# Performance work log

Measured on AMD Instinct MI355X. Metric: run time of the kernel, lower is better.

The kernel has to match this reference:

```python
import jax, jax.numpy as jnp
from jax import lax
import numpy as np

N_LAYER = 2
SEQ, BATCH, D = 4096, 32, 512


def setup_inputs() -> dict:
    key = jax.random.key(0)
    k1, k2, k3 = jax.random.split(key, 3)
    x = jax.random.normal(k1, (SEQ, BATCH, D), dtype=jnp.float32)
    # repo init: weight_ih ~ N(0, 0.01)
    W_ih = jax.random.normal(k2, (N_LAYER, D, D), dtype=jnp.float32) * 0.01
    # recurrent weight in [0,1) keeps the long ReLU recurrence bounded
    w_hh = jax.random.uniform(k3, (N_LAYER, D), dtype=jnp.float32)
    b_ih = jnp.zeros((N_LAYER, D), dtype=jnp.float32)
    return {"x": x, "W_ih": W_ih, "w_hh": w_hh, "b_ih": b_ih}


def _indrnn_layer(x, W, w, b):
    # x: (T, B, in), W: (H, in), w,b: (H,)
    proj = jnp.einsum('tbi,hi->tbh', x, W) + b  # one batched GEMM up front

    def step(h, p):
        h = jax.nn.relu(p + w * h)
        return h, h

    h0 = jnp.zeros((x.shape[1], W.shape[0]), dtype=x.dtype)
    hT, ys = lax.scan(step, h0, proj)
    return ys, hT


def reference(x, W_ih, w_hh, b_ih):
    hiddens = []
    out = x
    for l in range(W_ih.shape[0]):  # small fixed layer loop
        out, hT = _indrnn_layer(out, W_ih[l], w_hh[l], b_ih[l])
        hiddens.append(hT)
    h_n = jnp.stack(hiddens, axis=0)  # (n_layer, B, H)
    return out, h_n
```

## Files before the change

### kernel.cpp

```cpp
#include <hip/hip_runtime.h>

#define T_SEQ   4096
#define BATCH   32
#define DIM     512
#define MROWS   (T_SEQ * BATCH)
#define S_STRIDE (BATCH * DIM)
#define OUT_ELEMS ((size_t)T_SEQ * BATCH * DIM)
#define NCH     32
#define CLEN    (T_SEQ / NCH)
#define NCHAIN  (BATCH * DIM)

#define GNWG    ((MROWS / 256) * (DIM / 256))
#define OFF_A0  0
#define OFF_A1  16384
#define OFF_B0  32768
#define OFF_B1  49152
#define GLDS_B  131072

typedef __bf16 bf8_t __attribute__((ext_vector_type(8)));
typedef float  f4_t  __attribute__((ext_vector_type(4)));
typedef unsigned short u16x8 __attribute__((ext_vector_type(8)));
typedef __attribute__((address_space(1))) void gvoid_t;
typedef __attribute__((address_space(3))) void lvoid_t;

__device__ __forceinline__ unsigned short f2bf(float f) {
    unsigned int u = __float_as_uint(f);
    u += 0x7FFFu + ((u >> 16) & 1u);
    return (unsigned short)(u >> 16);
}
__device__ __forceinline__ float bf2f(unsigned short b) {
    return __uint_as_float(((unsigned int)b) << 16);
}

#define VMC(n)  asm volatile("s_waitcnt vmcnt(" #n ")" ::: "memory")
#define LGKM0   asm volatile("s_waitcnt lgkmcnt(0)" ::: "memory")
#define PH_PRE()  do { __builtin_amdgcn_s_barrier(); LGKM0;                    \
                       __builtin_amdgcn_sched_barrier(0);                      \
                       __builtin_amdgcn_s_setprio(1); } while (0)
#define PH_POST() do { __builtin_amdgcn_s_setprio(0);                          \
                       __builtin_amdgcn_sched_barrier(0);                      \
                       __builtin_amdgcn_s_barrier(); } while (0)

__global__ __launch_bounds__(256) void k_cvt(const float* __restrict__ in,
                                             unsigned short* __restrict__ out) {
    size_t i = ((size_t)blockIdx.x * 256 + threadIdx.x) * 8;
    float4 a = *reinterpret_cast<const float4*>(in + i);
    float4 b = *reinterpret_cast<const float4*>(in + i + 4);
    u16x8 o;
    o[0] = f2bf(a.x); o[1] = f2bf(a.y); o[2] = f2bf(a.z); o[3] = f2bf(a.w);
    o[4] = f2bf(b.x); o[5] = f2bf(b.y); o[6] = f2bf(b.z); o[7] = f2bf(b.w);
    *reinterpret_cast<u16x8*>(out + i) = o;
}

template <int AF32>
__global__ __launch_bounds__(512, 2)
void k_gemm8(const void* __restrict__ Ap,
             const unsigned short* __restrict__ Bp,
             unsigned short* __restrict__ C) {
    extern __shared__ unsigned short lds[];

    const int tid  = threadIdx.x;
    const int lane = tid & 63;
    const int wv   = tid >> 6;
    const int wr   = wv >> 2;
    const int wc   = wv & 3;
    const int l15  = lane & 15;
    const int l16  = lane >> 4;
    const int lj   = lane >> 3;
    const int ss8  = lane & 7;

    const int sid = (blockIdx.x & 7) * (GNWG / 8) + (blockIdx.x >> 3);
    const size_t gm = (size_t)(sid >> 1) * 256;
    const int    gn = (sid & 1) * 256;

    const unsigned short* Ab = (const unsigned short*)Ap;
    const float*          Af = (const float*)Ap;

    auto stage = [&](const unsigned short* gbase, size_t grow0, int region,
                     int half, int kt) {
#pragma unroll
        for (int j = 0; j < 2; ++j) {
            const int r = half * 128 + j * 64 + wv * 8 + lj;
            const unsigned short* src =
                gbase + (grow0 + r) * 512 + kt * 64 + ((ss8 ^ (r & 7)) * 8);
            unsigned short* dst = &lds[region + half * 8192 + j * 4096 + wv * 512];
            __builtin_amdgcn_global_load_lds((gvoid_t*)src, (lvoid_t*)dst, 16, 0, 0);
        }
    };
    auto loadAf = [&](float4* h, int half, int kt) {
#pragma unroll
        for (int j = 0; j < 2; ++j) {
            const int r = half * 128 + j * 64 + wv * 8 + lj;
            const float* src = Af + (gm + r) * 512 + kt * 64 + ss8 * 8;
            h[j * 2]     = *reinterpret_cast<const float4*>(src);
            h[j * 2 + 1] = *reinterpret_cast<const float4*>(src + 4);
        }
    };
    auto writeAf = [&](const float4* h, int region, int half) {
#pragma unroll
        for (int j = 0; j < 2; ++j) {
            const int r = half * 128 + j * 64 + wv * 8 + lj;
            float4 f0 = h[j * 2], f1 = h[j * 2 + 1];
            u16x8 o;
            o[0] = f2bf(f0.x); o[1] = f2bf(f0.y); o[2] = f2bf(f0.z); o[3] = f2bf(f0.w);
            o[4] = f2bf(f1.x); o[5] = f2bf(f1.y); o[6] = f2bf(f1.z); o[7] = f2bf(f1.w);
            *reinterpret_cast<u16x8*>(&lds[region + r * 64 + (ss8 ^ (r & 7)) * 8]) = o;
        }
    };

    f4_t  acc[8][4] = {};
    bf8_t bb[4][2];
    bf8_t aq[2][2];
    float4 afh0[4], afh1[4];

    auto loadBall = [&](int region) {
#pragma unroll
        for (int n = 0; n < 4; ++n)
#pragma unroll
            for (int ks = 0; ks < 2; ++ks) {
                const int c  = wc * 64 + n * 16 + l15;
                const int sl = (ks * 4 + l16) ^ (l15 & 7);
                bb[n][ks] = *reinterpret_cast<const bf8_t*>(
                    (const char*)&lds[region] + c * 128 + sl * 16);
            }
    };
    auto loadAq = [&](int region, int q) {
#pragma unroll
        for (int m = 0; m < 2; ++m)
#pragma unroll
            for (int ks = 0; ks < 2; ++ks) {
                const int r  = wr * 128 + (q * 2 + m) * 16 + l15;
                const int sl = (ks * 4 + l16) ^ (l15 & 7);
                aq[m][ks] = *reinterpret_cast<const bf8_t*>(
                    (const char*)&lds[region] + r * 128 + sl * 16);
            }
    };
#define MFMA_Q(q)                                                              \
    _Pragma("unroll")                                                          \
    for (int m = 0; m < 2; ++m)                                                \
        _Pragma("unroll")                                                      \
        for (int n = 0; n < 4; ++n)                                            \
            _Pragma("unroll")                                                  \
            for (int ks = 0; ks < 2; ++ks)                                     \
                acc[(q) * 2 + m][n] = __builtin_amdgcn_mfma_f32_16x16x32_bf16( \
                    aq[m][ks], bb[n][ks], acc[(q) * 2 + m][n], 0, 0, 0);

    if constexpr (AF32) {
        loadAf(afh0, 0, 0); loadAf(afh1, 1, 0);
        stage(Bp, (size_t)gn, OFF_B0, 0, 0); stage(Bp, (size_t)gn, OFF_B0, 1, 0);
        stage(Bp, (size_t)gn, OFF_B1, 0, 1); stage(Bp, (size_t)gn, OFF_B1, 1, 1);
        VMC(8);
        writeAf(afh0, OFF_A0, 0); writeAf(afh1, OFF_A0, 1);
        VMC(4);
        LGKM0;
    } else {
        stage(Ab, gm, OFF_A0, 0, 0); stage(Ab, gm, OFF_A0, 1, 0);
        stage(Bp, (size_t)gn, OFF_B0, 0, 0); stage(Bp, (size_t)gn, OFF_B0, 1, 0);
        stage(Bp, (size_t)gn, OFF_B1, 0, 1); stage(Bp, (size_t)gn, OFF_B1, 1, 1);
        VMC(4);
    }
    __builtin_amdgcn_s_barrier();

#pragma unroll
    for (int i = 0; i < 4; ++i) {
        const int t1 = 2 * i + 1, t2 = 2 * i + 2, t3 = 2 * i + 3;
        const bool st2 = (i < 3);

        loadBall(OFF_B0); loadAq(OFF_A0, 0);
        if constexpr (AF32) { loadAf(afh0, 0, t1); } else { stage(Ab, gm, OFF_A1, 0, t1); }
        PH_PRE(); MFMA_Q(0); PH_POST();
        loadAq(OFF_A0, 1);
        if constexpr (AF32) { loadAf(afh1, 1, t1); } else { stage(Ab, gm, OFF_A1, 1, t1); }
        PH_PRE(); MFMA_Q(1); PH_POST();
        loadAq(OFF_A0, 2);
        if (st2) stage(Bp, (size_t)gn, OFF_B0, 0, t2);
        PH_PRE(); MFMA_Q(2);
        __builtin_amdgcn_s_setprio(0); __builtin_amdgcn_sched_barrier(0);
        if constexpr (AF32) {
            if (st2) { VMC(6); } else { VMC(4); }
            writeAf(afh0, OFF_A1, 0);
        }
        __builtin_amdgcn_s_barrier();
        loadAq(OFF_A0, 3);
        if (st2) stage(Bp, (size_t)gn, OFF_B0, 1, t2);
        PH_PRE(); MFMA_Q(3);
        __builtin_amdgcn_s_setprio(0); __builtin_amdgcn_sched_barrier(0);
        if constexpr (AF32) {
            if (st2) { VMC(4); } else { VMC(0); }
            writeAf(afh1, OFF_A1, 1);
            LGKM0;
        } else {
            if (st2) { VMC(4); } else { VMC(0); }
        }
        __builtin_amdgcn_s_barrier();

        loadBall(OFF_B1); loadAq(OFF_A1, 0);
        if (st2) { if constexpr (AF32) { loadAf(afh0, 0, t2); } else { stage(Ab, gm, OFF_A0, 0, t2); } }
        PH_PRE(); MFMA_Q(0); PH_POST();
        loadAq(OFF_A1, 1);
        if (st2) { if constexpr (AF32) { loadAf(afh1, 1, t2); } else { stage(Ab, gm, OFF_A0, 1, t2); } }
        PH_PRE(); MFMA_Q(1); PH_POST();
        loadAq(OFF_A1, 2);
        if (st2) stage(Bp, (size_t)gn, OFF_B1, 0, t3);
        PH_PRE(); MFMA_Q(2);
        __builtin_amdgcn_s_setprio(0); __builtin_amdgcn_sched_barrier(0);
        if constexpr (AF32) { if (st2) { VMC(6); writeAf(afh0, OFF_A0, 0); } }
        __builtin_amdgcn_s_barrier();
        loadAq(OFF_A1, 3);
        if (st2) stage(Bp, (size_t)gn, OFF_B1, 1, t3);
        PH_PRE(); MFMA_Q(3);
        __builtin_amdgcn_s_setprio(0); __builtin_amdgcn_sched_barrier(0);
        if (st2) {
            VMC(4);
            if constexpr (AF32) { writeAf(afh1, OFF_A0, 1); LGKM0; }
        }
        __builtin_amdgcn_s_barrier();
    }
#undef MFMA_Q

    const int crow0 = l16 * 4;
#pragma unroll
    for (int m = 0; m < 8; ++m)
#pragma unroll
        for (int n = 0; n < 4; ++n) {
            const size_t row0 = gm + (size_t)(wr * 128 + m * 16 + crow0);
            const int    col  = gn + wc * 64 + n * 16 + l15;
#pragma unroll
            for (int r = 0; r < 4; ++r)
                C[(row0 + r) * 512 + col] = f2bf(acc[m][n][r]);
        }
}

__global__ __launch_bounds__(256)
void k_scan_p1(const unsigned short* __restrict__ q,
               const float* __restrict__ w_hh,
               const float* __restrict__ b_ih,
               float* __restrict__ Asum,
               float* __restrict__ Bsum) {
    const int g = (blockIdx.x & 63) * 256 + threadIdx.x;
    const int c = blockIdx.x >> 6;
    const float w  = w_hh[g & 511];
    const float bs = b_ih[g & 511];
    const unsigned short* p = q + (size_t)c * CLEN * S_STRIDE + g;

    float A = 0.f, Bv = 0.f;
    float s0[8], s1[8];
#pragma unroll
    for (int j = 0; j < 8; ++j) s0[j] = bf2f(p[(size_t)j * S_STRIDE]);
#pragma unroll
    for (int j = 0; j < 8; ++j) s1[j] = bf2f(p[(size_t)(8 + j) * S_STRIDE]);

    for (int j0 = 0; j0 < CLEN; j0 += 16) {
#pragma unroll
        for (int j = 0; j < 8; ++j) {
            float qv = s0[j] + bs;
            A  = fmaxf(fmaf(w, A, qv), 0.f);
            Bv = fmaf(w, Bv, qv);
        }
        if (j0 + 16 < CLEN) {
#pragma unroll
            for (int j = 0; j < 8; ++j) s0[j] = bf2f(p[(size_t)(j0 + 16 + j) * S_STRIDE]);
        }
#pragma unroll
        for (int j = 0; j < 8; ++j) {
            float qv = s1[j] + bs;
            A  = fmaxf(fmaf(w, A, qv), 0.f);
            Bv = fmaf(w, Bv, qv);
        }
        if (j0 + 24 < CLEN) {
#pragma unroll
            for (int j = 0; j < 8; ++j) s1[j] = bf2f(p[(size_t)(j0 + 24 + j) * S_STRIDE]);
        }
    }
    Asum[(size_t)c * NCHAIN + g] = A;
    Bsum[(size_t)c * NCHAIN + g] = Bv;
}

template <int MODE>
__global__ __launch_bounds__(256)
void k_scan_p2(const unsigned short* __restrict__ q,
               const float* __restrict__ w_hh,
               const float* __restrict__ b_ih,
               const float* __restrict__ Asum,
               const float* __restrict__ Bsum,
               float* __restrict__ of32,
               unsigned short* __restrict__ ob16,
               float* __restrict__ hT) {
    const int g = (blockIdx.x & 63) * 256 + threadIdx.x;
    const int c = blockIdx.x >> 6;
    const float w  = w_hh[g & 511];
    const float bs = b_ih[g & 511];

    float cw = w;
#pragma unroll
    for (int i = 0; i < 7; ++i) cw *= cw;
    float h = 0.f;
    for (int cc = 0; cc < c; ++cc)
        h = fmaxf(Asum[(size_t)cc * NCHAIN + g], fmaf(cw, h, Bsum[(size_t)cc * NCHAIN + g]));

    const size_t base = (size_t)c * CLEN * S_STRIDE + g;
    const unsigned short* p = q + base;

    float s0[8], s1[8];
#pragma unroll
    for (int j = 0; j < 8; ++j) s0[j] = bf2f(p[(size_t)j * S_STRIDE]);
#pragma unroll
    for (int j = 0; j < 8; ++j) s1[j] = bf2f(p[(size_t)(8 + j) * S_STRIDE]);

    for (int j0 = 0; j0 < CLEN; j0 += 16) {
#pragma unroll
        for (int j = 0; j < 8; ++j) {
            h = fmaxf(fmaf(w, h, s0[j] + bs), 0.f);
            const size_t idx = base + (size_t)(j0 + j) * S_STRIDE;
            if (MODE == 0) of32[idx] = h; else ob16[idx] = f2bf(h);
        }
        if (j0 + 16 < CLEN) {
#pragma unroll
            for (int j = 0; j < 8; ++j) s0[j] = bf2f(p[(size_t)(j0 + 16 + j) * S_STRIDE]);
        }
#pragma unroll
        for (int j = 0; j < 8; ++j) {
            h = fmaxf(fmaf(w, h, s1[j] + bs), 0.f);
            const size_t idx = base + (size_t)(j0 + 8 + j) * S_STRIDE;
            if (MODE == 0) of32[idx] = h; else ob16[idx] = f2bf(h);
        }
        if (j0 + 24 < CLEN) {
#pragma unroll
            for (int j = 0; j < 8; ++j) s1[j] = bf2f(p[(size_t)(j0 + 24 + j) * S_STRIDE]);
        }
    }
    if (c == NCH - 1) hT[g] = h;
}

extern "C" void kernel_launch(void* const* d_in, const int* in_sizes, int n_in,
                              void* d_out, int out_size, void* d_ws, size_t ws_size,
                              hipStream_t stream) {
    const float* x    = (const float*)d_in[0];
    const float* W_ih = (const float*)d_in[1];
    const float* w_hh = (const float*)d_in[2];
    const float* b_ih = (const float*)d_in[3];

    hipFuncSetAttribute(reinterpret_cast<const void*>(&k_gemm8<1>),
                        hipFuncAttributeMaxDynamicSharedMemorySize, GLDS_B);
    hipFuncSetAttribute(reinterpret_cast<const void*>(&k_gemm8<0>),
                        hipFuncAttributeMaxDynamicSharedMemorySize, GLDS_B);

    unsigned short* proj2 = (unsigned short*)d_ws;
    unsigned short* Wb    = proj2 + OUT_ELEMS;
    float* Asum = (float*)(Wb + 2 * 512 * 512);
    float* Bsum = Asum + (size_t)NCH * NCHAIN;

    unsigned short* proj1 = (unsigned short*)d_out;
    unsigned short* ys1   = proj1 + OUT_ELEMS;
    float* out = (float*)d_out;
    float* hT  = out + OUT_ELEMS;

    const int sgrid = 64 * NCH;

    k_cvt<<<524288 / 8 / 256, 256, 0, stream>>>(W_ih, Wb);
    k_gemm8<1><<<GNWG, 512, GLDS_B, stream>>>(x, Wb, proj1);
    k_scan_p1<<<sgrid, 256, 0, stream>>>(proj1, w_hh, b_ih, Asum, Bsum);
    k_scan_p2<1><<<sgrid, 256, 0, stream>>>(proj1, w_hh, b_ih, Asum, Bsum,
                                            nullptr, ys1, hT);
    k_gemm8<0><<<GNWG, 512, GLDS_B, stream>>>(ys1, Wb + 512 * 512, proj2);
    k_scan_p1<<<sgrid, 256, 0, stream>>>(proj2, w_hh + DIM, b_ih + DIM, Asum, Bsum);
    k_scan_p2<0><<<sgrid, 256, 0, stream>>>(proj2, w_hh + DIM, b_ih + DIM, Asum, Bsum,
                                            out, nullptr, hT + NCHAIN);
}
```

Baseline: 406.2 us.

## Make GEMM persistent over four M tiles with cross-tile prefetch

The projection GEMM now launches 256 persistent workgroups, one per CU, each covering four consecutive 256-row M tiles for a fixed N half. The last k-iteration of each tile prefetches the first A/B k-slices of the next tile, so the pipeline stays full across tile boundaries and the per-workgroup prologue and launch costs are paid once instead of per tile. Occupancy is reduced to one workgroup per CU (launch bounds 512,1), which gives up inter-workgroup latency hiding and relies on the intra-kernel software pipeline. The output stores of each tile remain unoverlapped with the next tile's compute.

```diff
diff --git a/kernel.cpp b/kernel.cpp
--- a/kernel.cpp
+++ b/kernel.cpp
@@ -10,7 +10,6 @@
 #define CLEN    (T_SEQ / NCH)
 #define NCHAIN  (BATCH * DIM)
 
-#define GNWG    ((MROWS / 256) * (DIM / 256))
 #define OFF_A0  0
 #define OFF_A1  16384
 #define OFF_B0  32768
@@ -53,10 +52,10 @@
 }
 
 template <int AF32>
-__global__ __launch_bounds__(512, 2)
-void k_gemm8(const void* __restrict__ Ap,
-             const unsigned short* __restrict__ Bp,
-             unsigned short* __restrict__ C) {
+__global__ __launch_bounds__(512, 1)
+void k_gemm8p(const void* __restrict__ Ap,
+              const unsigned short* __restrict__ Bp,
+              unsigned short* __restrict__ C) {
     extern __shared__ unsigned short lds[];
 
     const int tid  = threadIdx.x;
@@ -69,9 +68,10 @@
     const int lj   = lane >> 3;
     const int ss8  = lane & 7;
 
-    const int sid = (blockIdx.x & 7) * (GNWG / 8) + (blockIdx.x >> 3);
-    const size_t gm = (size_t)(sid >> 1) * 256;
-    const int    gn = (sid & 1) * 256;
+    const int nh = blockIdx.x >> 7;
+    const int mg = blockIdx.x & 127;
+    const int gn = nh * 256;
+    size_t gm = (size_t)mg * 1024;
 
     const unsigned short* Ab = (const unsigned short*)Ap;
     const float*          Af = (const float*)Ap;
@@ -87,11 +87,11 @@
             __builtin_amdgcn_global_load_lds((gvoid_t*)src, (lvoid_t*)dst, 16, 0, 0);
         }
     };
-    auto loadAf = [&](float4* h, int half, int kt) {
+    auto loadAf = [&](float4* h, int half, int kt, size_t gmx) {
 #pragma unroll
         for (int j = 0; j < 2; ++j) {
             const int r = half * 128 + j * 64 + wv * 8 + lj;
-            const float* src = Af + (gm + r) * 512 + kt * 64 + ss8 * 8;
+            const float* src = Af + (gmx + r) * 512 + kt * 64 + ss8 * 8;
             h[j * 2]     = *reinterpret_cast<const float4*>(src);
             h[j * 2 + 1] = *reinterpret_cast<const float4*>(src + 4);
         }
@@ -146,7 +146,7 @@
                     aq[m][ks], bb[n][ks], acc[(q) * 2 + m][n], 0, 0, 0);
 
     if constexpr (AF32) {
-        loadAf(afh0, 0, 0); loadAf(afh1, 1, 0);
+        loadAf(afh0, 0, 0, gm); loadAf(afh1, 1, 0, gm);
         stage(Bp, (size_t)gn, OFF_B0, 0, 0); stage(Bp, (size_t)gn, OFF_B0, 1, 0);
         stage(Bp, (size_t)gn, OFF_B1, 0, 1); stage(Bp, (size_t)gn, OFF_B1, 1, 1);
         VMC(8);
@@ -161,74 +161,85 @@
     }
     __builtin_amdgcn_s_barrier();
 
-#pragma unroll
-    for (int i = 0; i < 4; ++i) {
-        const int t1 = 2 * i + 1, t2 = 2 * i + 2, t3 = 2 * i + 3;
-        const bool st2 = (i < 3);
-
-        loadBall(OFF_B0); loadAq(OFF_A0, 0);
-        if constexpr (AF32) { loadAf(afh0, 0, t1); } else { stage(Ab, gm, OFF_A1, 0, t1); }
-        PH_PRE(); MFMA_Q(0); PH_POST();
-        loadAq(OFF_A0, 1);
-        if constexpr (AF32) { loadAf(afh1, 1, t1); } else { stage(Ab, gm, OFF_A1, 1, t1); }
-        PH_PRE(); MFMA_Q(1); PH_POST();
-        loadAq(OFF_A0, 2);
-        if (st2) stage(Bp, (size_t)gn, OFF_B0, 0, t2);
-        PH_PRE(); MFMA_Q(2);
-        __builtin_amdgcn_s_setprio(0); __builtin_amdgcn_sched_barrier(0);
-        if constexpr (AF32) {
-            if (st2) { VMC(6); } else { VMC(4); }
-            writeAf(afh0, OFF_A1, 0);
-        }
-        __builtin_amdgcn_s_barrier();
-        loadAq(OFF_A0, 3);
-        if (st2) stage(Bp, (size_t)gn, OFF_B0, 1, t2);
-        PH_PRE(); MFMA_Q(3);
-        __builtin_amdgcn_s_setprio(0); __builtin_amdgcn_sched_barrier(0);
-        if constexpr (AF32) {
-            if (st2) { VMC(4); } else { VMC(0); }
-            writeAf(afh1, OFF_A1, 1);
-            LGKM0;
-        } else {
-            if (st2) { VMC(4); } else { VMC(0); }
-        }
-        __builtin_amdgcn_s_barrier();
-
-        loadBall(OFF_B1); loadAq(OFF_A1, 0);
-        if (st2) { if constexpr (AF32) { loadAf(afh0, 0, t2); } else { stage(Ab, gm, OFF_A0, 0, t2); } }
-        PH_PRE(); MFMA_Q(0); PH_POST();
-        loadAq(OFF_A1, 1);
-        if (st2) { if constexpr (AF32) { loadAf(afh1, 1, t2); } else { stage(Ab, gm, OFF_A0, 1, t2); } }
-        PH_PRE(); MFMA_Q(1); PH_POST();
-        loadAq(OFF_A1, 2);
-        if (st2) stage(Bp, (size_t)gn, OFF_B1, 0, t3);
-        PH_PRE(); MFMA_Q(2);
-        __builtin_amdgcn_s_setprio(0); __builtin_amdgcn_sched_barrier(0);
-        if constexpr (AF32) { if (st2) { VMC(6); writeAf(afh0, OFF_A0, 0); } }
-        __builtin_amdgcn_s_barrier();
-        loadAq(OFF_A1, 3);
-        if (st2) stage(Bp, (size_t)gn, OFF_B1, 1, t3);
-        PH_PRE(); MFMA_Q(3);
-        __builtin_amdgcn_s_setprio(0); __builtin_amdgcn_sched_barrier(0);
-        if (st2) {
-            VMC(4);
-            if constexpr (AF32) { writeAf(afh1, OFF_A0, 1); LGKM0; }
-        }
-        __builtin_amdgcn_s_barrier();
+    for (int jb = 0; jb < 4; ++jb) {
+        const size_t gmN = gm + 256;
+        const bool   nx  = (jb < 3);
+
+#pragma unroll
+        for (int i = 0; i < 4; ++i) {
+            const int    t1   = 2 * i + 1;
+            const bool   last = (i == 3);
+            const int    kt2  = last ? 0 : 2 * i + 2;
+            const int    kt3  = last ? 1 : 2 * i + 3;
+            const size_t g2   = last ? gmN : gm;
+            const bool   st2  = (!last) || nx;
+
+            loadBall(OFF_B0); loadAq(OFF_A0, 0);
+            if constexpr (AF32) { loadAf(afh0, 0, t1, gm); } else { stage(Ab, gm, OFF_A1, 0, t1); }
+            PH_PRE(); MFMA_Q(0); PH_POST();
+            loadAq(OFF_A0, 1);
+            if constexpr (AF32) { loadAf(afh1, 1, t1, gm); } else { stage(Ab, gm, OFF_A1, 1, t1); }
+            PH_PRE(); MFMA_Q(1); PH_POST();
+            loadAq(OFF_A0, 2);
+            if (st2) stage(Bp, (size_t)gn, OFF_B0, 0, kt2);
+            PH_PRE(); MFMA_Q(2);
+            __builtin_amdgcn_s_setprio(0); __builtin_amdgcn_sched_barrier(0);
+            if constexpr (AF32) {
+                if (st2) { VMC(6); } else { VMC(4); }
+                writeAf(afh0, OFF_A1, 0);
+            }
+            __builtin_amdgcn_s_barrier();
+            loadAq(OFF_A0, 3);
+            if (st2) stage(Bp, (size_t)gn, OFF_B0, 1, kt2);
+            PH_PRE(); MFMA_Q(3);
+            __builtin_amdgcn_s_setprio(0); __builtin_amdgcn_sched_barrier(0);
+            if constexpr (AF32) {
+                if (st2) { VMC(4); } else { VMC(0); }
+                writeAf(afh1, OFF_A1, 1);
+                LGKM0;
+            } else {
+                if (st2) { VMC(4); } else { VMC(0); }
+            }
+            __builtin_amdgcn_s_barrier();
+
+            loadBall(OFF_B1); loadAq(OFF_A1, 0);
+            if (st2) { if constexpr (AF32) { loadAf(afh0, 0, kt2, g2); } else { stage(Ab, g2, OFF_A0, 0, kt2); } }
+            PH_PRE(); MFMA_Q(0); PH_POST();
+            loadAq(OFF_A1, 1);
+            if (st2) { if constexpr (AF32) { loadAf(afh1, 1, kt2, g2); } else { stage(Ab, g2, OFF_A0, 1, kt2); } }
+            PH_PRE(); MFMA_Q(1); PH_POST();
+            loadAq(OFF_A1, 2);
+            if (st2) stage(Bp, (size_t)gn, OFF_B1, 0, kt3);
+            PH_PRE(); MFMA_Q(2);
+            __builtin_amdgcn_s_setprio(0); __builtin_amdgcn_sched_barrier(0);
+            if constexpr (AF32) { if (st2) { VMC(6); writeAf(afh0, OFF_A0, 0); } }
+            __builtin_amdgcn_s_barrier();
+            loadAq(OFF_A1, 3);
+            if (st2) stage(Bp, (size_t)gn, OFF_B1, 1, kt3);
+            PH_PRE(); MFMA_Q(3);
+            __builtin_amdgcn_s_setprio(0); __builtin_amdgcn_sched_barrier(0);
+            if (st2) {
+                VMC(4);
+                if constexpr (AF32) { writeAf(afh1, OFF_A0, 1); LGKM0; }
+            }
+            __builtin_amdgcn_s_barrier();
+        }
+
+        const int crow0 = l16 * 4;
+#pragma unroll
+        for (int m = 0; m < 8; ++m)
+#pragma unroll
+            for (int n = 0; n < 4; ++n) {
+                const size_t row0 = gm + (size_t)(wr * 128 + m * 16 + crow0);
+                const int    col  = gn + wc * 64 + n * 16 + l15;
+#pragma unroll
+                for (int r = 0; r < 4; ++r)
+                    C[(row0 + r) * 512 + col] = f2bf(acc[m][n][r]);
+                acc[m][n] = (f4_t){0.f, 0.f, 0.f, 0.f};
+            }
+        gm = gmN;
     }
 #undef MFMA_Q
-
-    const int crow0 = l16 * 4;
-#pragma unroll
-    for (int m = 0; m < 8; ++m)
-#pragma unroll
-        for (int n = 0; n < 4; ++n) {
-            const size_t row0 = gm + (size_t)(wr * 128 + m * 16 + crow0);
-            const int    col  = gn + wc * 64 + n * 16 + l15;
-#pragma unroll
-            for (int r = 0; r < 4; ++r)
-                C[(row0 + r) * 512 + col] = f2bf(acc[m][n][r]);
-        }
 }
 
 __global__ __launch_bounds__(256)
@@ -340,9 +351,9 @@
     const float* w_hh = (const float*)d_in[2];
     const float* b_ih = (const float*)d_in[3];
 
-    hipFuncSetAttribute(reinterpret_cast<const void*>(&k_gemm8<1>),
+    hipFuncSetAttribute(reinterpret_cast<const void*>(&k_gemm8p<1>),
                         hipFuncAttributeMaxDynamicSharedMemorySize, GLDS_B);
-    hipFuncSetAttribute(reinterpret_cast<const void*>(&k_gemm8<0>),
+    hipFuncSetAttribute(reinterpret_cast<const void*>(&k_gemm8p<0>),
                         hipFuncAttributeMaxDynamicSharedMemorySize, GLDS_B);
 
     unsigned short* proj2 = (unsigned short*)d_ws;
@@ -358,11 +369,11 @@
     const int sgrid = 64 * NCH;
 
     k_cvt<<<524288 / 8 / 256, 256, 0, stream>>>(W_ih, Wb);
-    k_gemm8<1><<<GNWG, 512, GLDS_B, stream>>>(x, Wb, proj1);
+    k_gemm8p<1><<<256, 512, GLDS_B, stream>>>(x, Wb, proj1);
     k_scan_p1<<<sgrid, 256, 0, stream>>>(proj1, w_hh, b_ih, Asum, Bsum);
     k_scan_p2<1><<<sgrid, 256, 0, stream>>>(proj1, w_hh, b_ih, Asum, Bsum,
                                             nullptr, ys1, hT);
-    k_gemm8<0><<<GNWG, 512, GLDS_B, stream>>>(ys1, Wb + 512 * 512, proj2);
+    k_gemm8p<0><<<256, 512, GLDS_B, stream>>>(ys1, Wb + 512 * 512, proj2);
     k_scan_p1<<<sgrid, 256, 0, stream>>>(proj2, w_hh + DIM, b_ih + DIM, Asum, Bsum);
     k_scan_p2<0><<<sgrid, 256, 0, stream>>>(proj2, w_hh + DIM, b_ih + DIM, Asum, Bsum,
                                             out, nullptr, hT + NCHAIN);
```

After: 627.8 us. 54.6% more time.
